# Kernel tuning notes

Hardware: AMD Instinct MI355X
Metric: run time of the kernel (lower is better)

## Reference

```python
import jax, jax.numpy as jnp
import numpy as np

N_NODES = 50000
N_EDGES = 1_600_000
D = 128


def setup_inputs() -> dict:
    key = jax.random.key(0)
    k1, k2, k3 = jax.random.split(key, 3)
    x = jax.random.normal(k1, (N_NODES, D), dtype=jnp.float32)
    edge_index = jax.random.randint(k2, (2, N_EDGES), 0, N_NODES, dtype=jnp.int64)
    W = jax.random.normal(k3, (D, D), dtype=jnp.float32) / np.sqrt(D)
    b = jnp.zeros((D,), dtype=jnp.float32)
    return {"x": x, "edge_index": edge_index, "W": W, "b": b}


def _sgconv(x, src, dst, W, b, n):
    # gcn_norm with self-loops: D^{-1/2} (A + I) D^{-1/2}
    loop = jnp.arange(n, dtype=src.dtype)
    src = jnp.concatenate([src, loop])
    dst = jnp.concatenate([dst, loop])
    ones = jnp.ones(src.shape[0], dtype=x.dtype)
    deg = jax.ops.segment_sum(ones, dst, num_segments=n)  # in-degree incl. self-loop
    dinv = jnp.where(deg > 0, jax.lax.rsqrt(deg), jnp.zeros_like(deg))
    norm = dinv[src] * dinv[dst]                      # [E+N]
    msg = x[src] * norm[:, None]                      # gather + scale, [E+N, D]
    agg = jax.ops.segment_sum(msg, dst, num_segments=n)  # scatter-add, [N, D]
    return agg @ W.T + b                              # SGConv linear (K=1)


def reference(x, edge_index, W, b):
    n = x.shape[0]
    h = _sgconv(x, edge_index[0], edge_index[1], W, b, n)
    return x + jax.nn.relu(h)
```

## Files before the change

kernel.cpp:

```cpp
#include <hip/hip_runtime.h>
#include <hip/hip_fp16.h>

#define D 128
#define BSHIFT 6
#define BSIZE 64
#define NBMAX 1024
#define BCAP 3072
#define PA_BLOCKS 256
#define OVF_CAP 65536
#define GB_THREADS 1024

using half8 = __attribute__((ext_vector_type(8))) _Float16;
using float4v = __attribute__((ext_vector_type(4))) float;

__global__ __launch_bounds__(256) void histA_kernel(const int* __restrict__ dst,
                                                    int* __restrict__ ph, int E, int NB) {
    __shared__ int hist[NBMAX];
    int t = threadIdx.x;
    for (int b = t; b < NB; b += 256) hist[b] = 0;
    __syncthreads();
    int chunk = (((E + (int)gridDim.x - 1) / (int)gridDim.x) + 3) & ~3;
    int start = blockIdx.x * chunk;
    int end = min(start + chunk, E);
    for (int i = start + 4 * t; i < end; i += 4 * 256) {
        if (i + 3 < end) {
            int4 v = *(const int4*)&dst[i];
            atomicAdd(&hist[v.x >> BSHIFT], 1);
            atomicAdd(&hist[v.y >> BSHIFT], 1);
            atomicAdd(&hist[v.z >> BSHIFT], 1);
            atomicAdd(&hist[v.w >> BSHIFT], 1);
        } else {
            for (int j = i; j < end; ++j) atomicAdd(&hist[dst[j] >> BSHIFT], 1);
        }
    }
    __syncthreads();
    int* row = ph + (size_t)blockIdx.x * NB;
    for (int b = t; b < NB; b += 256) row[b] = hist[b];
}

__global__ __launch_bounds__(PA_BLOCKS) void scanA_kernel(int* __restrict__ ph,
                                                          int* __restrict__ bucket_cnt,
                                                          int NB) {
    __shared__ int sh[PA_BLOCKS];
    int b = blockIdx.x;
    int t = threadIdx.x;
    int v = ph[(size_t)t * NB + b];
    sh[t] = v;
    __syncthreads();
    for (int off = 1; off < PA_BLOCKS; off <<= 1) {
        int add = (t >= off) ? sh[t - off] : 0;
        __syncthreads();
        sh[t] += add;
        __syncthreads();
    }
    ph[(size_t)t * NB + b] = sh[t] - v;
    if (t == PA_BLOCKS - 1) bucket_cnt[b] = sh[t];
}

__global__ __launch_bounds__(256) void placeA_kernel(const int* __restrict__ src,
                                                     const int* __restrict__ dst,
                                                     const int* __restrict__ ph,
                                                     int* __restrict__ pairs,
                                                     int* __restrict__ ovfA_cnt,
                                                     int2* __restrict__ ovfA,
                                                     int E, int NB) {
    __shared__ int sbase[NBMAX];
    __shared__ int cur[NBMAX];
    int t = threadIdx.x;
    const int* row = ph + (size_t)blockIdx.x * NB;
    for (int b = t; b < NB; b += 256) { sbase[b] = row[b]; cur[b] = 0; }
    __syncthreads();
    int chunk = (((E + (int)gridDim.x - 1) / (int)gridDim.x) + 3) & ~3;
    int start = blockIdx.x * chunk;
    int end = min(start + chunk, E);

    auto place = [&](int dd, int ss) {
        int b = dd >> BSHIFT;
        int p = sbase[b] + atomicAdd(&cur[b], 1);
        if (p < BCAP) {
            pairs[(size_t)b * BCAP + p] = (ss << BSHIFT) | (dd & (BSIZE - 1));
        } else {
            int q = atomicAdd(ovfA_cnt, 1);
            if (q < OVF_CAP) ovfA[q] = make_int2(dd, ss);
        }
    };

    for (int i = start + 4 * t; i < end; i += 4 * 256) {
        if (i + 3 < end) {
            int4 dv = *(const int4*)&dst[i];
            int4 sv = *(const int4*)&src[i];
            place(dv.x, sv.x);
            place(dv.y, sv.y);
            place(dv.z, sv.z);
            place(dv.w, sv.w);
        } else {
            for (int j = i; j < end; ++j) place(dst[j], src[j]);
        }
    }
}

__global__ __launch_bounds__(256) void degB_kernel(const int* __restrict__ pairs,
                                                   const int* __restrict__ bucket_cnt,
                                                   const int* __restrict__ ovfA_cnt,
                                                   const int2* __restrict__ ovfA,
                                                   float* __restrict__ dinv, int N) {
    __shared__ int degL[BSIZE];
    int b = blockIdx.x, t = threadIdx.x;
    if (t < BSIZE) degL[t] = 0;
    __syncthreads();
    int cnt = min(bucket_cnt[b], BCAP);
    const int* pp = pairs + (size_t)b * BCAP;
    for (int i = t; i < cnt; i += 256) atomicAdd(&degL[pp[i] & (BSIZE - 1)], 1);
    int na = *ovfA_cnt;
    if (na > 0) {
        if (na > OVF_CAP) na = OVF_CAP;
        for (int k = t; k < na; k += 256) {
            int dd = ovfA[k].x;
            if ((dd >> BSHIFT) == b) atomicAdd(&degL[dd & (BSIZE - 1)], 1);
        }
    }
    __syncthreads();
    if (t < BSIZE) {
        int node = b * BSIZE + t;
        if (node < N) dinv[node] = rsqrtf((float)degL[t] + 1.0f);
    }
}

__global__ __launch_bounds__(256) void xw_kernel(const float* __restrict__ x,
                                                 const float* __restrict__ dinv,
                                                 const float* __restrict__ W,
                                                 __half* __restrict__ xw, int N) {
    __shared__ _Float16 Bf[128 * 128];
    const int t = threadIdx.x;
    {
        int n = t >> 1;
        int jt = n >> 4, nlo = n & 15;
        int kbase = (t & 1) * 64;
#pragma unroll
        for (int o = 0; o < 8; ++o) {
            int k0 = kbase + o * 8;
            float4 f0 = *(const float4*)&W[n * 128 + k0];
            float4 f1 = *(const float4*)&W[n * 128 + k0 + 4];
            int kt = k0 >> 5, quad = (k0 >> 3) & 3;
            half8 h;
            h[0] = (_Float16)f0.x; h[1] = (_Float16)f0.y;
            h[2] = (_Float16)f0.z; h[3] = (_Float16)f0.w;
            h[4] = (_Float16)f1.x; h[5] = (_Float16)f1.y;
            h[6] = (_Float16)f1.z; h[7] = (_Float16)f1.w;
            *(half8*)&Bf[(size_t)(((kt * 8 + jt) * 4 + quad) * 16 + nlo) * 8] = h;
        }
    }
    __syncthreads();

    const int wave = t >> 6, lane = t & 63;
    const int quad = lane >> 4, nlo = lane & 15;
    const int r0 = blockIdx.x * 64 + wave * 16;
    const int rA = r0 + nlo;
    const int rAc = (rA < N) ? rA : (N - 1);
    const float dv = dinv[rAc];

    float4v acc[8];
#pragma unroll
    for (int j = 0; j < 8; ++j) acc[j] = (float4v){0.f, 0.f, 0.f, 0.f};

#pragma unroll
    for (int kt = 0; kt < 4; ++kt) {
        const float* xp = x + (size_t)rAc * D + kt * 32 + quad * 8;
        float4 a0 = *(const float4*)xp;
        float4 a1 = *(const float4*)(xp + 4);
        half8 va;
        va[0] = (_Float16)(a0.x * dv); va[1] = (_Float16)(a0.y * dv);
        va[2] = (_Float16)(a0.z * dv); va[3] = (_Float16)(a0.w * dv);
        va[4] = (_Float16)(a1.x * dv); va[5] = (_Float16)(a1.y * dv);
        va[6] = (_Float16)(a1.z * dv); va[7] = (_Float16)(a1.w * dv);
#pragma unroll
        for (int jt = 0; jt < 8; ++jt) {
            half8 vb = *(half8*)&Bf[(size_t)((kt * 8 + jt) * 64 + lane) * 8];
            acc[jt] = __builtin_amdgcn_mfma_f32_16x16x32_f16(va, vb, acc[jt], 0, 0, 0);
        }
    }

#pragma unroll
    for (int reg = 0; reg < 4; ++reg) {
        int row = r0 + quad * 4 + reg;
        if (row < N) {
            half8 h;
#pragma unroll
            for (int jt = 0; jt < 8; ++jt) h[jt] = (_Float16)acc[jt][reg];
            *(half8*)((_Float16*)xw + (size_t)row * D + nlo * 8) = h;
        }
    }
}

__global__ __launch_bounds__(GB_THREADS) void gatherB_kernel(
    const float* __restrict__ x, const __half* __restrict__ xw,
    const int* __restrict__ pairs, const int* __restrict__ bucket_cnt,
    const float* __restrict__ dinv, const float* __restrict__ bias,
    const int* __restrict__ ovfA_cnt, const int2* __restrict__ ovfA,
    float* __restrict__ out, int N) {
    __shared__ int lds_src[BCAP];
    __shared__ int degL[BSIZE], offs[BSIZE], cur[BSIZE];
    const int b = blockIdx.x;
    const int t = threadIdx.x;
    if (t < BSIZE) { degL[t] = 0; cur[t] = 0; }
    __syncthreads();
    const int cnt = min(bucket_cnt[b], BCAP);

    int my_w[3], my_n = 0;
    for (int i = t; i < cnt; i += GB_THREADS) {
        int w = pairs[(size_t)b * BCAP + i];
        my_w[my_n++] = w;
        atomicAdd(&degL[w & (BSIZE - 1)], 1);
    }
    __syncthreads();

    if (t < BSIZE) {
        int v = degL[t];
        int s = v;
#pragma unroll
        for (int o = 1; o < 64; o <<= 1) {
            int u = __shfl_up(s, o, 64);
            if (t >= o) s += u;
        }
        offs[t] = s - v;
    }
    __syncthreads();

    for (int k = 0; k < my_n; ++k) {
        int w = my_w[k];
        int dl = w & (BSIZE - 1);
        int p = atomicAdd(&cur[dl], 1);
        lds_src[offs[dl] + p] = w >> BSHIFT;
    }
    __syncthreads();

    const int wave = t >> 6, lane = t & 63;
    const __half2* xw2 = (const __half2*)xw;
    int na = *ovfA_cnt;
    if (na > OVF_CAP) na = OVF_CAP;

    for (int q = 0; q < 4; ++q) {
        int dl = wave * 4 + q;
        int node = b * BSIZE + dl;
        if (node >= N) break;
        int start = offs[dl];
        int end = start + degL[dl];
        float dvd = dinv[node];
        size_t noff = (size_t)node * D;

        float2 fs = __half22float2(xw2[(size_t)node * 64 + lane]);
        float s0 = fs.x, s1 = fs.y;

        int e = start;
        for (; e + 7 < end; e += 8) {
            int i0 = lds_src[e + 0], i1 = lds_src[e + 1];
            int i2 = lds_src[e + 2], i3 = lds_src[e + 3];
            int i4 = lds_src[e + 4], i5 = lds_src[e + 5];
            int i6 = lds_src[e + 6], i7 = lds_src[e + 7];
            float2 f0 = __half22float2(xw2[(size_t)i0 * 64 + lane]);
            float2 f1 = __half22float2(xw2[(size_t)i1 * 64 + lane]);
            float2 f2 = __half22float2(xw2[(size_t)i2 * 64 + lane]);
            float2 f3 = __half22float2(xw2[(size_t)i3 * 64 + lane]);
            float2 f4 = __half22float2(xw2[(size_t)i4 * 64 + lane]);
            float2 f5 = __half22float2(xw2[(size_t)i5 * 64 + lane]);
            float2 f6 = __half22float2(xw2[(size_t)i6 * 64 + lane]);
            float2 f7 = __half22float2(xw2[(size_t)i7 * 64 + lane]);
            s0 += (f0.x + f1.x) + (f2.x + f3.x) + ((f4.x + f5.x) + (f6.x + f7.x));
            s1 += (f0.y + f1.y) + (f2.y + f3.y) + ((f4.y + f5.y) + (f6.y + f7.y));
        }
        for (; e < end; ++e) {
            float2 f = __half22float2(xw2[(size_t)lds_src[e] * 64 + lane]);
            s0 += f.x;
            s1 += f.y;
        }

        if (na > 0) {
            for (int k = 0; k < na; ++k) {
                int2 pr = ovfA[k];
                if (pr.x == node) {
                    float2 f = __half22float2(xw2[(size_t)pr.y * 64 + lane]);
                    s0 += f.x; s1 += f.y;
                }
            }
        }

        int c0 = (lane & 3) * 32 + (lane >> 2);
        int c1 = c0 + 16;
        float h0 = s0 * dvd + bias[c0];
        float h1 = s1 * dvd + bias[c1];
        out[noff + c0] = x[noff + c0] + (h0 > 0.f ? h0 : 0.f);
        out[noff + c1] = x[noff + c1] + (h1 > 0.f ? h1 : 0.f);
    }
}

extern "C" void kernel_launch(void* const* d_in, const int* in_sizes, int n_in,
                              void* d_out, int out_size, void* d_ws, size_t ws_size,
                              hipStream_t stream) {
    const float* x = (const float*)d_in[0];
    const int* ei = (const int*)d_in[1];
    const float* W = (const float*)d_in[2];
    const float* bias = (const float*)d_in[3];
    float* out = (float*)d_out;

    const int N = in_sizes[0] / D;
    const int E = in_sizes[1] / 2;
    const int* src = ei;
    const int* dst = ei + E;
    const int NB = (N + BSIZE - 1) / BSIZE;

    char* p = (char*)d_ws;
    int* pairs = (int*)p;      p += (size_t)NB * BCAP * sizeof(int);
    __half* xw = (__half*)p;   p += (size_t)N * D * sizeof(__half);
    float* dinv = (float*)p;   p += (size_t)N * sizeof(float);
    int* bucket_cnt = (int*)p; p += (size_t)NBMAX * sizeof(int);
    int* ovfA_cnt = (int*)p;   p += 16;
    int2* ovfA = (int2*)p;     p += (size_t)OVF_CAP * sizeof(int2);
    int* ph = (int*)p;         p += (size_t)PA_BLOCKS * NB * sizeof(int);

    hipMemsetAsync(ovfA_cnt, 0, 16, stream);

    histA_kernel<<<PA_BLOCKS, 256, 0, stream>>>(dst, ph, E, NB);
    scanA_kernel<<<NB, PA_BLOCKS, 0, stream>>>(ph, bucket_cnt, NB);
    placeA_kernel<<<PA_BLOCKS, 256, 0, stream>>>(src, dst, ph, pairs,
                                                 ovfA_cnt, ovfA, E, NB);
    degB_kernel<<<NB, 256, 0, stream>>>(pairs, bucket_cnt, ovfA_cnt, ovfA, dinv, N);
    xw_kernel<<<(N + 63) / 64, 256, 0, stream>>>(x, dinv, W, xw, N);
    gatherB_kernel<<<NB, GB_THREADS, 0, stream>>>(x, xw, pairs, bucket_cnt,
                                                  dinv, bias, ovfA_cnt, ovfA,
                                                  out, N);
}
```

Before: 185.8 us.

## Store transformed features as FP8 and fold degree computation into xw kernel

Removes the separate degree kernel: xw_kernel computes per-bucket in-degrees in LDS and derives dinv itself, and gatherB recomputes dinv from its own degree counts plus overflow counts. The intermediate xw is stored as FP8 instead of FP16, halving the bytes moved by the random gather. The gather loop now splits each wave into two halves that read different edges with 4-byte loads and combine partial sums with a cross-lane shuffle. FP8 storage lowers precision of the aggregated messages, which may exceed tolerance.

```diff
diff --git a/kernel.cpp b/kernel.cpp
--- a/kernel.cpp
+++ b/kernel.cpp
@@ -12,6 +12,7 @@
 
 using half8 = __attribute__((ext_vector_type(8))) _Float16;
 using float4v = __attribute__((ext_vector_type(4))) float;
+using floatx2 = __attribute__((ext_vector_type(2))) float;
 
 __global__ __launch_bounds__(256) void histA_kernel(const int* __restrict__ dst,
                                                     int* __restrict__ ph, int E, int NB) {
@@ -99,39 +100,34 @@
     }
 }
 
-__global__ __launch_bounds__(256) void degB_kernel(const int* __restrict__ pairs,
-                                                   const int* __restrict__ bucket_cnt,
-                                                   const int* __restrict__ ovfA_cnt,
-                                                   const int2* __restrict__ ovfA,
-                                                   float* __restrict__ dinv, int N) {
-    __shared__ int degL[BSIZE];
-    int b = blockIdx.x, t = threadIdx.x;
-    if (t < BSIZE) degL[t] = 0;
-    __syncthreads();
-    int cnt = min(bucket_cnt[b], BCAP);
-    const int* pp = pairs + (size_t)b * BCAP;
-    for (int i = t; i < cnt; i += 256) atomicAdd(&degL[pp[i] & (BSIZE - 1)], 1);
-    int na = *ovfA_cnt;
-    if (na > 0) {
-        if (na > OVF_CAP) na = OVF_CAP;
-        for (int k = t; k < na; k += 256) {
-            int dd = ovfA[k].x;
-            if ((dd >> BSHIFT) == b) atomicAdd(&degL[dd & (BSIZE - 1)], 1);
-        }
-    }
-    __syncthreads();
-    if (t < BSIZE) {
-        int node = b * BSIZE + t;
-        if (node < N) dinv[node] = rsqrtf((float)degL[t] + 1.0f);
-    }
-}
-
 __global__ __launch_bounds__(256) void xw_kernel(const float* __restrict__ x,
-                                                 const float* __restrict__ dinv,
                                                  const float* __restrict__ W,
-                                                 __half* __restrict__ xw, int N) {
+                                                 const int* __restrict__ pairs,
+                                                 const int* __restrict__ bucket_cnt,
+                                                 const int* __restrict__ ovfA_cnt,
+                                                 const int2* __restrict__ ovfA,
+                                                 unsigned char* __restrict__ xw, int N) {
     __shared__ _Float16 Bf[128 * 128];
+    __shared__ int degX[BSIZE];
     const int t = threadIdx.x;
+    const int b = blockIdx.x;
+    if (t < BSIZE) degX[t] = 0;
+    __syncthreads();
+
+    {
+        int cnt = min(bucket_cnt[b], BCAP);
+        const int* pp = pairs + (size_t)b * BCAP;
+        for (int i = t; i < cnt; i += 256) atomicAdd(&degX[pp[i] & (BSIZE - 1)], 1);
+        int na = *ovfA_cnt;
+        if (na > 0) {
+            if (na > OVF_CAP) na = OVF_CAP;
+            for (int k = t; k < na; k += 256) {
+                int dd = ovfA[k].x;
+                if ((dd >> BSHIFT) == b) atomicAdd(&degX[dd & (BSIZE - 1)], 1);
+            }
+        }
+    }
+
     {
         int n = t >> 1;
         int jt = n >> 4, nlo = n & 15;
@@ -154,10 +150,10 @@
 
     const int wave = t >> 6, lane = t & 63;
     const int quad = lane >> 4, nlo = lane & 15;
-    const int r0 = blockIdx.x * 64 + wave * 16;
+    const int r0 = b * 64 + wave * 16;
     const int rA = r0 + nlo;
     const int rAc = (rA < N) ? rA : (N - 1);
-    const float dv = dinv[rAc];
+    const float dv = rsqrtf((float)degX[rAc - b * 64] + 1.0f);
 
     float4v acc[8];
 #pragma unroll
@@ -184,27 +180,29 @@
     for (int reg = 0; reg < 4; ++reg) {
         int row = r0 + quad * 4 + reg;
         if (row < N) {
-            half8 h;
-#pragma unroll
-            for (int jt = 0; jt < 8; ++jt) h[jt] = (_Float16)acc[jt][reg];
-            *(half8*)((_Float16*)xw + (size_t)row * D + nlo * 8) = h;
+            int u0 = __builtin_amdgcn_cvt_pk_fp8_f32(acc[0][reg], acc[1][reg], 0, false);
+            u0 = __builtin_amdgcn_cvt_pk_fp8_f32(acc[2][reg], acc[3][reg], u0, true);
+            int u1 = __builtin_amdgcn_cvt_pk_fp8_f32(acc[4][reg], acc[5][reg], 0, false);
+            u1 = __builtin_amdgcn_cvt_pk_fp8_f32(acc[6][reg], acc[7][reg], u1, true);
+            *(uint2*)(xw + (size_t)row * 128 + nlo * 8) = make_uint2((unsigned)u0, (unsigned)u1);
         }
     }
 }
 
 __global__ __launch_bounds__(GB_THREADS) void gatherB_kernel(
-    const float* __restrict__ x, const __half* __restrict__ xw,
+    const float* __restrict__ x, const unsigned char* __restrict__ xw,
     const int* __restrict__ pairs, const int* __restrict__ bucket_cnt,
-    const float* __restrict__ dinv, const float* __restrict__ bias,
-    const int* __restrict__ ovfA_cnt, const int2* __restrict__ ovfA,
-    float* __restrict__ out, int N) {
+    const float* __restrict__ bias, const int* __restrict__ ovfA_cnt,
+    const int2* __restrict__ ovfA, float* __restrict__ out, int N) {
     __shared__ int lds_src[BCAP];
-    __shared__ int degL[BSIZE], offs[BSIZE], cur[BSIZE];
+    __shared__ int degL[BSIZE], offs[BSIZE], cur[BSIZE], spillc[BSIZE];
     const int b = blockIdx.x;
     const int t = threadIdx.x;
-    if (t < BSIZE) { degL[t] = 0; cur[t] = 0; }
+    if (t < BSIZE) { degL[t] = 0; cur[t] = 0; spillc[t] = 0; }
     __syncthreads();
     const int cnt = min(bucket_cnt[b], BCAP);
+    int na = *ovfA_cnt;
+    if (na > OVF_CAP) na = OVF_CAP;
 
     int my_w[3], my_n = 0;
     for (int i = t; i < cnt; i += GB_THREADS) {
@@ -212,6 +210,12 @@
         my_w[my_n++] = w;
         atomicAdd(&degL[w & (BSIZE - 1)], 1);
     }
+    if (na > 0) {
+        for (int k = t; k < na; k += GB_THREADS) {
+            int dd = ovfA[k].x;
+            if ((dd >> BSHIFT) == b) atomicAdd(&spillc[dd & (BSIZE - 1)], 1);
+        }
+    }
     __syncthreads();
 
     if (t < BSIZE) {
@@ -235,9 +239,17 @@
     __syncthreads();
 
     const int wave = t >> 6, lane = t & 63;
-    const __half2* xw2 = (const __half2*)xw;
-    int na = *ovfA_cnt;
-    if (na > OVF_CAP) na = OVF_CAP;
+    const int half = lane >> 5, c31 = lane & 31;
+    const unsigned int* xw32 = (const unsigned int*)xw;
+
+    int col[4];
+    float bcol[4];
+#pragma unroll
+    for (int k = 0; k < 4; ++k) {
+        int s = 4 * c31 + k;
+        col[k] = ((s & 7) << 4) + (s >> 3);
+        bcol[k] = bias[col[k]];
+    }
 
     for (int q = 0; q < 4; ++q) {
         int dl = wave * 4 + q;
@@ -245,51 +257,77 @@
         if (node >= N) break;
         int start = offs[dl];
         int end = start + degL[dl];
-        float dvd = dinv[node];
+        float dvd = rsqrtf((float)(degL[dl] + spillc[dl]) + 1.0f);
         size_t noff = (size_t)node * D;
 
-        float2 fs = __half22float2(xw2[(size_t)node * 64 + lane]);
-        float s0 = fs.x, s1 = fs.y;
+        float a0 = 0.f, a1 = 0.f, a2 = 0.f, a3 = 0.f;
 
         int e = start;
         for (; e + 7 < end; e += 8) {
-            int i0 = lds_src[e + 0], i1 = lds_src[e + 1];
-            int i2 = lds_src[e + 2], i3 = lds_src[e + 3];
-            int i4 = lds_src[e + 4], i5 = lds_src[e + 5];
-            int i6 = lds_src[e + 6], i7 = lds_src[e + 7];
-            float2 f0 = __half22float2(xw2[(size_t)i0 * 64 + lane]);
-            float2 f1 = __half22float2(xw2[(size_t)i1 * 64 + lane]);
-            float2 f2 = __half22float2(xw2[(size_t)i2 * 64 + lane]);
-            float2 f3 = __half22float2(xw2[(size_t)i3 * 64 + lane]);
-            float2 f4 = __half22float2(xw2[(size_t)i4 * 64 + lane]);
-            float2 f5 = __half22float2(xw2[(size_t)i5 * 64 + lane]);
-            float2 f6 = __half22float2(xw2[(size_t)i6 * 64 + lane]);
-            float2 f7 = __half22float2(xw2[(size_t)i7 * 64 + lane]);
-            s0 += (f0.x + f1.x) + (f2.x + f3.x) + ((f4.x + f5.x) + (f6.x + f7.x));
-            s1 += (f0.y + f1.y) + (f2.y + f3.y) + ((f4.y + f5.y) + (f6.y + f7.y));
-        }
-        for (; e < end; ++e) {
-            float2 f = __half22float2(xw2[(size_t)lds_src[e] * 64 + lane]);
-            s0 += f.x;
-            s1 += f.y;
-        }
-
-        if (na > 0) {
-            for (int k = 0; k < na; ++k) {
-                int2 pr = ovfA[k];
-                if (pr.x == node) {
-                    float2 f = __half22float2(xw2[(size_t)pr.y * 64 + lane]);
-                    s0 += f.x; s1 += f.y;
+            int r0 = lds_src[e + 0 + half], r1 = lds_src[e + 2 + half];
+            int r2 = lds_src[e + 4 + half], r3 = lds_src[e + 6 + half];
+            unsigned int w0 = xw32[(size_t)r0 * 32 + c31];
+            unsigned int w1 = xw32[(size_t)r1 * 32 + c31];
+            unsigned int w2 = xw32[(size_t)r2 * 32 + c31];
+            unsigned int w3 = xw32[(size_t)r3 * 32 + c31];
+            floatx2 l0 = __builtin_amdgcn_cvt_pk_f32_fp8((int)w0, false);
+            floatx2 h0 = __builtin_amdgcn_cvt_pk_f32_fp8((int)w0, true);
+            floatx2 l1 = __builtin_amdgcn_cvt_pk_f32_fp8((int)w1, false);
+            floatx2 h1 = __builtin_amdgcn_cvt_pk_f32_fp8((int)w1, true);
+            floatx2 l2 = __builtin_amdgcn_cvt_pk_f32_fp8((int)w2, false);
+            floatx2 h2 = __builtin_amdgcn_cvt_pk_f32_fp8((int)w2, true);
+            floatx2 l3 = __builtin_amdgcn_cvt_pk_f32_fp8((int)w3, false);
+            floatx2 h3 = __builtin_amdgcn_cvt_pk_f32_fp8((int)w3, true);
+            a0 += (l0.x + l1.x) + (l2.x + l3.x);
+            a1 += (l0.y + l1.y) + (l2.y + l3.y);
+            a2 += (h0.x + h1.x) + (h2.x + h3.x);
+            a3 += (h0.y + h1.y) + (h2.y + h3.y);
+        }
+        for (; e + 1 < end; e += 2) {
+            int r = lds_src[e + half];
+            unsigned int w = xw32[(size_t)r * 32 + c31];
+            floatx2 lo = __builtin_amdgcn_cvt_pk_f32_fp8((int)w, false);
+            floatx2 hi = __builtin_amdgcn_cvt_pk_f32_fp8((int)w, true);
+            a0 += lo.x; a1 += lo.y; a2 += hi.x; a3 += hi.y;
+        }
+        if (e < end && half == 0) {
+            int r = lds_src[e];
+            unsigned int w = xw32[(size_t)r * 32 + c31];
+            floatx2 lo = __builtin_amdgcn_cvt_pk_f32_fp8((int)w, false);
+            floatx2 hi = __builtin_amdgcn_cvt_pk_f32_fp8((int)w, true);
+            a0 += lo.x; a1 += lo.y; a2 += hi.x; a3 += hi.y;
+        }
+
+        a0 += __shfl_xor(a0, 32);
+        a1 += __shfl_xor(a1, 32);
+        a2 += __shfl_xor(a2, 32);
+        a3 += __shfl_xor(a3, 32);
+
+        if (half == 0) {
+            unsigned int ws = xw32[(size_t)node * 32 + c31];
+            floatx2 lo = __builtin_amdgcn_cvt_pk_f32_fp8((int)ws, false);
+            floatx2 hi = __builtin_amdgcn_cvt_pk_f32_fp8((int)ws, true);
+            a0 += lo.x; a1 += lo.y; a2 += hi.x; a3 += hi.y;
+            if (na > 0) {
+                for (int k = 0; k < na; ++k) {
+                    int2 pr = ovfA[k];
+                    if (pr.x == node) {
+                        unsigned int w = xw32[(size_t)pr.y * 32 + c31];
+                        floatx2 l2_ = __builtin_amdgcn_cvt_pk_f32_fp8((int)w, false);
+                        floatx2 h2_ = __builtin_amdgcn_cvt_pk_f32_fp8((int)w, true);
+                        a0 += l2_.x; a1 += l2_.y; a2 += h2_.x; a3 += h2_.y;
+                    }
                 }
             }
-        }
-
-        int c0 = (lane & 3) * 32 + (lane >> 2);
-        int c1 = c0 + 16;
-        float h0 = s0 * dvd + bias[c0];
-        float h1 = s1 * dvd + bias[c1];
-        out[noff + c0] = x[noff + c0] + (h0 > 0.f ? h0 : 0.f);
-        out[noff + c1] = x[noff + c1] + (h1 > 0.f ? h1 : 0.f);
+            float h0 = a0 * dvd + bcol[0];
+            float h1 = a1 * dvd + bcol[1];
+            float h2 = a2 * dvd + bcol[2];
+            float h3 = a3 * dvd + bcol[3];
+            out[noff + col[0]] = x[noff + col[0]] + (h0 > 0.f ? h0 : 0.f);
+            out[noff + col[1]] = x[noff + col[1]] + (h1 > 0.f ? h1 : 0.f);
+            out[noff + col[2]] = x[noff + col[2]] + (h2 > 0.f ? h2 : 0.f);
+            out[noff + col[3]] = x[noff + col[3]] + (h3 > 0.f ? h3 : 0.f);
+        }
     }
 }
 
@@ -309,13 +347,12 @@
     const int NB = (N + BSIZE - 1) / BSIZE;
 
     char* p = (char*)d_ws;
-    int* pairs = (int*)p;      p += (size_t)NB * BCAP * sizeof(int);
-    __half* xw = (__half*)p;   p += (size_t)N * D * sizeof(__half);
-    float* dinv = (float*)p;   p += (size_t)N * sizeof(float);
-    int* bucket_cnt = (int*)p; p += (size_t)NBMAX * sizeof(int);
-    int* ovfA_cnt = (int*)p;   p += 16;
-    int2* ovfA = (int2*)p;     p += (size_t)OVF_CAP * sizeof(int2);
-    int* ph = (int*)p;         p += (size_t)PA_BLOCKS * NB * sizeof(int);
+    int* pairs = (int*)p;            p += (size_t)NB * BCAP * sizeof(int);
+    unsigned char* xw = (unsigned char*)p; p += (size_t)N * 128;
+    int* bucket_cnt = (int*)p;       p += (size_t)NBMAX * sizeof(int);
+    int* ovfA_cnt = (int*)p;         p += 16;
+    int2* ovfA = (int2*)p;           p += (size_t)OVF_CAP * sizeof(int2);
+    int* ph = (int*)p;               p += (size_t)PA_BLOCKS * NB * sizeof(int);
 
     hipMemsetAsync(ovfA_cnt, 0, 16, stream);
 
@@ -323,9 +360,7 @@
     scanA_kernel<<<NB, PA_BLOCKS, 0, stream>>>(ph, bucket_cnt, NB);
     placeA_kernel<<<PA_BLOCKS, 256, 0, stream>>>(src, dst, ph, pairs,
                                                  ovfA_cnt, ovfA, E, NB);
-    degB_kernel<<<NB, 256, 0, stream>>>(pairs, bucket_cnt, ovfA_cnt, ovfA, dinv, N);
-    xw_kernel<<<(N + 63) / 64, 256, 0, stream>>>(x, dinv, W, xw, N);
+    xw_kernel<<<NB, 256, 0, stream>>>(x, W, pairs, bucket_cnt, ovfA_cnt, ovfA, xw, N);
     gatherB_kernel<<<NB, GB_THREADS, 0, stream>>>(x, xw, pairs, bucket_cnt,
-                                                  dinv, bias, ovfA_cnt, ovfA,
-                                                  out, N);
-}
+                                                  bias, ovfA_cnt, ovfA, out, N);
+}
```

Result: faster. 160.3 us (-13.7%).
